# Performance work log

Hardware: AMD Instinct MI355X
Metric: run time of the kernel (lower is better)

Reference implementation:

```python
import jax, jax.numpy as jnp
import numpy as np

N_NODES = 100000
N_EDGES = 1600000
IN_DIM, HID, OUT_DIM = 128, 64, 1


def _sage_conv(x, src, dst, wl, wr, b, num_nodes):
    # PyG SAGEConv (aggr='mean', root_weight=True):
    #   out = lin_l(mean_{j in N(i)} x_j) + lin_r(x_i), bias lives in lin_l
    msgs = x[src]                                                  # [E, d] gather
    agg = jax.ops.segment_sum(msgs, dst, num_segments=num_nodes)  # [N, d]
    deg = jax.ops.segment_sum(jnp.ones((src.shape[0],), x.dtype), dst,
                              num_segments=num_nodes)              # [N]
    agg = agg / jnp.maximum(deg, 1.0)[:, None]                     # mean aggregation
    return agg @ wl + x @ wr + b


def setup_inputs() -> dict:
    key = jax.random.key(0)
    ks = jax.random.split(key, 12)
    x = jax.random.normal(ks[0], (N_NODES, IN_DIM), dtype=jnp.float32)
    edge_index = jax.random.randint(ks[1], (2, N_EDGES), 0, N_NODES, dtype=jnp.int64)

    def glorot(k, fan_in, fan_out):
        s = jnp.sqrt(2.0 / (fan_in + fan_out)).astype(jnp.float32)
        return jax.random.normal(k, (fan_in, fan_out), dtype=jnp.float32) * s

    return {
        "x": x,
        "edge_index": edge_index,
        "wl0": glorot(ks[2], IN_DIM, HID), "wr0": glorot(ks[3], IN_DIM, HID),
        "b0": jnp.zeros((HID,), jnp.float32),
        "wl1": glorot(ks[4], HID, HID), "wr1": glorot(ks[5], HID, HID),
        "b1": jnp.zeros((HID,), jnp.float32),
        "wl2": glorot(ks[6], HID, OUT_DIM), "wr2": glorot(ks[7], HID, OUT_DIM),
        "b2": jnp.zeros((OUT_DIM,), jnp.float32),
    }


def reference(x, edge_index, wl0, wr0, b0, wl1, wr1, b1, wl2, wr2, b2):
    src, dst = edge_index[0], edge_index[1]
    n = x.shape[0]
    # layer 0: conv -> relu (dropout is identity in eval mode)
    h = jax.nn.relu(_sage_conv(x, src, dst, wl0, wr0, b0, n))
    # layer 1
    h = jax.nn.relu(_sage_conv(h, src, dst, wl1, wr1, b1, n))
    # final layer + sigmoid
    h = _sage_conv(h, src, dst, wl2, wr2, b2, n)
    return jax.nn.sigmoid(h)
```

## Files before the change

### kernel.cpp

```cpp
#include <hip/hip_runtime.h>
#include <hip/hip_bf16.h>
#include <math.h>


#define SHIFT 7
#define BKT 128
#define CHUNK 4096

typedef __bf16 bf16_t;
typedef bf16_t bf16x8 __attribute__((ext_vector_type(8)));
typedef float f32x4 __attribute__((ext_vector_type(4)));

__global__ __launch_bounds__(256) void hist_bucket(const int* __restrict__ dstv,
                                                   int* __restrict__ bucket_cnt,
                                                   int E, int NB, int nbC,
                                                   const float* __restrict__ wl0,
                                                   const float* __restrict__ wr0,
                                                   const float* __restrict__ wl1,
                                                   const float* __restrict__ wr1,
                                                   bf16_t* __restrict__ w0t,
                                                   bf16_t* __restrict__ w1t) {
    if ((int)blockIdx.x >= nbC) {
        int idx = (blockIdx.x - nbC) * 256 + threadIdx.x;
        if (idx < 128 * 128) {
            int j = idx >> 7, k = idx & 127;
            float v = (j < 64) ? wl0[k * 64 + j] : wr0[k * 64 + (j - 64)];
            w0t[idx] = (bf16_t)v;
        } else if (idx < 128 * 128 + 128 * 64) {
            int i2 = idx - 128 * 128;
            int j = i2 >> 6, k = i2 & 63;
            float v = (j < 64) ? wl1[k * 64 + j] : wr1[k * 64 + (j - 64)];
            w1t[i2] = (bf16_t)v;
        }
        return;
    }
    __shared__ int h[1024];
    for (int i = threadIdx.x; i < NB; i += 256) h[i] = 0;
    __syncthreads();
    int base = blockIdx.x * CHUNK;
#pragma unroll
    for (int k = 0; k < CHUNK / 256; ++k) {
        int e = base + threadIdx.x + k * 256;
        if (e < E) atomicAdd(&h[dstv[e] >> SHIFT], 1);
    }
    __syncthreads();
    for (int i = threadIdx.x; i < NB; i += 256)
        if (h[i]) atomicAdd(&bucket_cnt[i], h[i]);
}

__global__ __launch_bounds__(1024) void scan_bucket(const int* __restrict__ cnt,
                                                    int* __restrict__ boff,
                                                    int* __restrict__ bcur, int NB) {
    __shared__ int s[1024];
    int t = threadIdx.x;
    int v = (t < NB) ? cnt[t] : 0;
    s[t] = v;
    __syncthreads();
    for (int d = 1; d < 1024; d <<= 1) {
        int x = (t >= d) ? s[t - d] : 0;
        __syncthreads();
        s[t] += x;
        __syncthreads();
    }
    if (t < NB) {
        int o = s[t] - v;
        boff[t] = o;
        bcur[t] = o;
    }
    if (t == NB - 1) boff[NB] = s[t];
}

__global__ __launch_bounds__(256) void scatter_bucket(const int* __restrict__ srcv,
                                                      const int* __restrict__ dstv,
                                                      int* __restrict__ bcur,
                                                      int* __restrict__ bucketed,
                                                      int E, int NB) {
    __shared__ int hist[1024];
    __shared__ int offl[1024];
    __shared__ int basel[1024];
    __shared__ int partial[256];
    __shared__ int posA[CHUNK];
    __shared__ int valA[CHUNK];
    const int t = threadIdx.x;
    for (int i = t; i < NB; i += 256) hist[i] = 0;
    __syncthreads();

    const int cbase = blockIdx.x * CHUNK;
    int bk[CHUNK / 256], rk[CHUNK / 256], vv[CHUNK / 256];
#pragma unroll
    for (int k = 0; k < CHUNK / 256; ++k) {
        int e = cbase + t + k * 256;
        if (e < E) {
            int d = dstv[e];
            int s = srcv[e];
            int b = d >> SHIFT;
            bk[k] = b;
            rk[k] = atomicAdd(&hist[b], 1);
            vv[k] = (s << SHIFT) | (d & (BKT - 1));
        } else {
            bk[k] = -1;
        }
    }
    __syncthreads();

    for (int b = t; b < NB; b += 256) {
        int c = hist[b];
        basel[b] = c ? atomicAdd(&bcur[b], c) : 0;
    }
    {
        int g = t * 4;
        int a0 = (g + 0 < NB) ? hist[g + 0] : 0;
        int a1 = (g + 1 < NB) ? hist[g + 1] : 0;
        int a2 = (g + 2 < NB) ? hist[g + 2] : 0;
        int a3 = (g + 3 < NB) ? hist[g + 3] : 0;
        int sum = a0 + a1 + a2 + a3;
        partial[t] = sum;
        __syncthreads();
        for (int d = 1; d < 256; d <<= 1) {
            int x = (t >= d) ? partial[t - d] : 0;
            __syncthreads();
            partial[t] += x;
            __syncthreads();
        }
        int ex = partial[t] - sum;
        if (g + 0 < NB) offl[g + 0] = ex;
        if (g + 1 < NB) offl[g + 1] = ex + a0;
        if (g + 2 < NB) offl[g + 2] = ex + a0 + a1;
        if (g + 3 < NB) offl[g + 3] = ex + a0 + a1 + a2;
    }
    __syncthreads();

    int nloc = E - cbase;
    if (nloc > CHUNK) nloc = CHUNK;
#pragma unroll
    for (int k = 0; k < CHUNK / 256; ++k) {
        if (bk[k] >= 0) {
            int slot = offl[bk[k]] + rk[k];
            posA[slot] = basel[bk[k]] + rk[k];
            valA[slot] = vv[k];
        }
    }
    __syncthreads();
    for (int j = t; j < nloc; j += 256) bucketed[posA[j]] = valA[j];
}

__global__ __launch_bounds__(256) void sort_bucket(const int* __restrict__ bucketed,
                                                   const int* __restrict__ boff,
                                                   int2* __restrict__ od,
                                                   int* __restrict__ csr, int N) {
    __shared__ int cnt[BKT];
    __shared__ int sc[BKT];
    __shared__ int cur[BKT];
    const int b = blockIdx.x;
    const int t = threadIdx.x;
    const int ebase = boff[b], eend = boff[b + 1];
    if (t < BKT) cnt[t] = 0;
    __syncthreads();
    for (int i = ebase + t; i < eend; i += 256)
        atomicAdd(&cnt[bucketed[i] & (BKT - 1)], 1);
    __syncthreads();
    int v = (t < BKT) ? cnt[t] : 0;
    if (t < BKT) sc[t] = v;
    __syncthreads();
    for (int d = 1; d < BKT; d <<= 1) {
        int x = (t < BKT && t >= d) ? sc[t - d] : 0;
        __syncthreads();
        if (t < BKT) sc[t] += x;
        __syncthreads();
    }
    if (t < BKT) {
        int ex = sc[t] - v;
        cur[t] = ex;
        int dst = (b << SHIFT) + t;
        if (dst < N) od[dst] = make_int2(ebase + ex, v);
    }
    __syncthreads();
    for (int i = ebase + t; i < eend; i += 256) {
        int w = bucketed[i];
        int p = atomicAdd(&cur[w & (BKT - 1)], 1);
        csr[ebase + p] = w >> SHIFT;
    }
}

template <int KTOT, bool AIN_BF16>
__global__ __launch_bounds__(256) void gemm_mfma(const void* __restrict__ Ain,
                                                 const bf16_t* __restrict__ Wt,
                                                 bf16_t* __restrict__ Y, int N) {
    const int lane = threadIdx.x & 63;
    const int wv = threadIdx.x >> 6;
    const int r0 = blockIdx.x * 64 + wv * 16;
    const int rr = lane & 15;
    const int quad = lane >> 4;
    const int row_store = r0 + rr;
    int row = (row_store < N) ? row_store : (N - 1);
    constexpr int NK = KTOT / 32;

    bf16x8 xf[NK];
    if (AIN_BF16) {
        const bf16_t* A = (const bf16_t*)Ain;
#pragma unroll
        for (int kk = 0; kk < NK; ++kk)
            xf[kk] = *(const bf16x8*)&A[(size_t)row * KTOT + kk * 32 + quad * 8];
    } else {
        const float* A = (const float*)Ain;
#pragma unroll
        for (int kk = 0; kk < NK; ++kk) {
            const float* ap = &A[(size_t)row * KTOT + kk * 32 + quad * 8];
            float4 f0 = *(const float4*)ap;
            float4 f1 = *(const float4*)(ap + 4);
            union { bf16x8 v; bf16_t h[8]; } u;
            u.h[0] = (bf16_t)f0.x; u.h[1] = (bf16_t)f0.y;
            u.h[2] = (bf16_t)f0.z; u.h[3] = (bf16_t)f0.w;
            u.h[4] = (bf16_t)f1.x; u.h[5] = (bf16_t)f1.y;
            u.h[6] = (bf16_t)f1.z; u.h[7] = (bf16_t)f1.w;
            xf[kk] = u.v;
        }
    }

#pragma unroll
    for (int c = 0; c < 8; ++c) {
        f32x4 acc = {0.f, 0.f, 0.f, 0.f};
#pragma unroll
        for (int kk = 0; kk < NK; ++kk) {
            bf16x8 wf = *(const bf16x8*)&Wt[(size_t)(c * 16 + rr) * KTOT + kk * 32 + quad * 8];
            acc = __builtin_amdgcn_mfma_f32_16x16x32_bf16(wf, xf[kk], acc, 0, 0, 0);
        }
        if (row_store < N) {
            union { bf16_t h[4]; uint2 u; } p;
            p.h[0] = (bf16_t)acc[0]; p.h[1] = (bf16_t)acc[1];
            p.h[2] = (bf16_t)acc[2]; p.h[3] = (bf16_t)acc[3];
            *(uint2*)&Y[(size_t)row_store * 128 + c * 16 + quad * 4] = p.u;
        }
    }
}

template <bool FUSED>
__global__ __launch_bounds__(256) void agg_relu(const bf16_t* __restrict__ y,
                                                const int* __restrict__ csr,
                                                const int2* __restrict__ od,
                                                const float* __restrict__ bias,
                                                bf16_t* __restrict__ h,
                                                const float* __restrict__ wl2,
                                                const float* __restrict__ wr2,
                                                float* __restrict__ sl,
                                                float* __restrict__ sr, int N) {
    int wid = blockIdx.x * 4 + (threadIdx.x >> 6);
    if (wid >= N) return;
    const int lane = threadIdx.x & 63;
    const int half = lane >> 5;
    const int ch = (lane & 31) * 2;
    const int2 odv = od[wid];
    const int base = odv.x;
    const int d = odv.y;

    int sidx = (lane < d) ? csr[base + lane] : 0;

    int lastLane = (d > 0 && d - 1 < 64) ? (d - 1) : 0;
    int s_last = __shfl(sidx, lastLane);

    float ax = 0.f, ay = 0.f;
    const int npairs = d >> 1;
    const int pm = (npairs < 32) ? npairs : 32;
    int p = 0;
    for (; p + 8 <= pm; p += 8) {
        int s[8];
#pragma unroll
        for (int j = 0; j < 8; ++j) s[j] = __shfl(sidx, 2 * (p + j) + half);
        uint v[8];
#pragma unroll
        for (int j = 0; j < 8; ++j) v[j] = *(const uint*)&y[(size_t)s[j] * 128 + ch];
#pragma unroll
        for (int j = 0; j < 8; ++j) {
            ax += __uint_as_float(v[j] << 16);
            ay += __uint_as_float(v[j] & 0xffff0000u);
        }
    }
    for (; p < pm; ++p) {
        int s0 = __shfl(sidx, 2 * p + half);
        uint v0 = *(const uint*)&y[(size_t)s0 * 128 + ch];
        ax += __uint_as_float(v0 << 16);
        ay += __uint_as_float(v0 & 0xffff0000u);
    }
    for (; p < npairs; ++p) {
        int s0 = csr[base + 2 * p + half];
        uint v0 = *(const uint*)&y[(size_t)s0 * 128 + ch];
        ax += __uint_as_float(v0 << 16);
        ay += __uint_as_float(v0 & 0xffff0000u);
    }
    if ((d & 1) && half == 0) {
        int s0 = (d - 1 < 64) ? s_last : csr[base + d - 1];
        uint v0 = *(const uint*)&y[(size_t)s0 * 128 + ch];
        ax += __uint_as_float(v0 << 16);
        ay += __uint_as_float(v0 & 0xffff0000u);
    }
    ax += __shfl_xor(ax, 32);
    ay += __shfl_xor(ay, 32);

    float inv = 1.f / ((d > 0) ? (float)d : 1.f);
    uint vs = *(const uint*)&y[(size_t)wid * 128 + 64 + ch];
    float2 bv = *(const float2*)&bias[ch];
    float vx = fmaxf(ax * inv + __uint_as_float(vs << 16) + bv.x, 0.f);
    float vy = fmaxf(ay * inv + __uint_as_float(vs & 0xffff0000u) + bv.y, 0.f);

    if (!FUSED) {
        if (half == 0) {
            union { bf16_t b[2]; uint u; } pk;
            pk.b[0] = (bf16_t)vx;
            pk.b[1] = (bf16_t)vy;
            *(uint*)&h[(size_t)wid * 64 + ch] = pk.u;
        }
    } else {
        float a = vx * wl2[ch] + vy * wl2[ch + 1];
        float b = vx * wr2[ch] + vy * wr2[ch + 1];
#pragma unroll
        for (int off = 16; off; off >>= 1) {
            a += __shfl_xor(a, off);
            b += __shfl_xor(b, off);
        }
        if (lane == 0) {
            sl[wid] = a;
            sr[wid] = b;
        }
    }
}

__global__ __launch_bounds__(256) void final_k(const float* __restrict__ sl,
                                               const float* __restrict__ sr,
                                               const int* __restrict__ csr,
                                               const int2* __restrict__ od,
                                               const float* __restrict__ b2,
                                               float* __restrict__ out, int N) {
    int wid = blockIdx.x * 4 + (threadIdx.x >> 6);
    if (wid >= N) return;
    const int lane = threadIdx.x & 63;
    const int2 odv = od[wid];
    const int base = odv.x;
    const int d = odv.y;
    float acc = 0.f;
    for (int e = lane; e < d; e += 64) acc += sl[csr[base + e]];
#pragma unroll
    for (int off = 32; off; off >>= 1) acc += __shfl_xor(acc, off);
    if (lane == 0) {
        float m = (d > 0) ? (float)d : 1.f;
        float v = acc / m + sr[wid] + b2[0];
        out[wid] = 1.f / (1.f + expf(-v));
    }
}

extern "C" void kernel_launch(void* const* d_in, const int* in_sizes, int n_in,
                              void* d_out, int out_size, void* d_ws, size_t ws_size,
                              hipStream_t stream) {
    const float* x  = (const float*)d_in[0];
    const int*  ei  = (const int*)d_in[1];
    const float* wl0 = (const float*)d_in[2];
    const float* wr0 = (const float*)d_in[3];
    const float* b0  = (const float*)d_in[4];
    const float* wl1 = (const float*)d_in[5];
    const float* wr1 = (const float*)d_in[6];
    const float* b1  = (const float*)d_in[7];
    const float* wl2 = (const float*)d_in[8];
    const float* wr2 = (const float*)d_in[9];
    const float* b2  = (const float*)d_in[10];
    float* out = (float*)d_out;

    const int E = in_sizes[1] / 2;
    const int N = out_size;
    const int* srcv = ei;
    const int* dstv = ei + E;
    const int NB = (N + BKT - 1) >> SHIFT;

    char* ws = (char*)d_ws;
    size_t o = 0;
    auto take = [&](size_t nbytes) -> void* {
        void* p = ws + o;
        o = (o + nbytes + 255) & ~(size_t)255;
        return p;
    };
    int2* od    = (int2*)take((size_t)N * 8);
    int* bcnt   = (int*)take((size_t)(NB + 2) * 4);
    int* boff   = (int*)take((size_t)(NB + 2) * 4);
    int* bcur   = (int*)take((size_t)(NB + 2) * 4);
    int* csr    = (int*)take((size_t)E * 4);
    bf16_t* w0t = (bf16_t*)take(128 * 128 * 2);
    bf16_t* w1t = (bf16_t*)take(128 * 64 * 2);
    bf16_t* y   = (bf16_t*)take((size_t)N * 128 * 2);
    bf16_t* h   = (bf16_t*)take((size_t)N * 64 * 2);
    float* sl   = (float*)take((size_t)N * 4);
    float* sr   = (float*)take((size_t)N * 4);
    int* bucketed = (int*)y;
    (void)ws_size;

    const int nbC = (E + CHUNK - 1) / CHUNK;
    const int nbP = (128 * 128 + 128 * 64 + 255) / 256;
    const int nbW = (N + 3) / 4;
    const int nbG = (N + 63) / 64;

    hipMemsetAsync(bcnt, 0, (size_t)NB * 4, stream);
    hist_bucket<<<nbC + nbP, 256, 0, stream>>>(dstv, bcnt, E, NB, nbC,
                                               wl0, wr0, wl1, wr1, w0t, w1t);
    scan_bucket<<<1, 1024, 0, stream>>>(bcnt, boff, bcur, NB);
    scatter_bucket<<<nbC, 256, 0, stream>>>(srcv, dstv, bcur, bucketed, E, NB);
    sort_bucket<<<NB, 256, 0, stream>>>(bucketed, boff, od, csr, N);

    gemm_mfma<128, false><<<nbG, 256, 0, stream>>>((const void*)x, w0t, y, N);
    agg_relu<false><<<nbW, 256, 0, stream>>>(y, csr, od, b0, h,
                                             nullptr, nullptr, nullptr, nullptr, N);
    gemm_mfma<64, true><<<nbG, 256, 0, stream>>>((const void*)h, w1t, y, N);
    agg_relu<true><<<nbW, 256, 0, stream>>>(y, csr, od, b1, nullptr,
                                            wl2, wr2, sl, sr, N);
    final_k<<<nbW, 256, 0, stream>>>(sl, sr, csr, od, b2, out, N);
}
```

Baseline: 330.7 us.

## Use persistent grid-stride waves with 4 edges per step and prefetched CSR indices in aggregation

Rewrites agg_relu as a persistent kernel on 2048 blocks where each wave loops over nodes in grid-stride order. While it aggregates the current node, it prefetches the next node's offset/degree and neighbor indices. Lanes now split into quads that each handle one edge with 8-byte loads of 4 channels, so four edges are in flight per step instead of two. This aims to hide index-load latency and issue wider gathers. The cost is an extra cross-quad shuffle reduction and less parallelism per node.

```diff
diff --git a/kernel.cpp b/kernel.cpp
--- a/kernel.cpp
+++ b/kernel.cpp
@@ -234,6 +234,9 @@
     }
 }
 
+#define B16LO(u) __uint_as_float((u) << 16)
+#define B16HI(u) __uint_as_float((u) & 0xffff0000u)
+
 template <bool FUSED>
 __global__ __launch_bounds__(256) void agg_relu(const bf16_t* __restrict__ y,
                                                 const int* __restrict__ csr,
@@ -244,83 +247,106 @@
                                                 const float* __restrict__ wr2,
                                                 float* __restrict__ sl,
                                                 float* __restrict__ sr, int N) {
-    int wid = blockIdx.x * 4 + (threadIdx.x >> 6);
-    if (wid >= N) return;
     const int lane = threadIdx.x & 63;
-    const int half = lane >> 5;
-    const int ch = (lane & 31) * 2;
-    const int2 odv = od[wid];
-    const int base = odv.x;
-    const int d = odv.y;
-
-    int sidx = (lane < d) ? csr[base + lane] : 0;
-
-    int lastLane = (d > 0 && d - 1 < 64) ? (d - 1) : 0;
-    int s_last = __shfl(sidx, lastLane);
-
-    float ax = 0.f, ay = 0.f;
-    const int npairs = d >> 1;
-    const int pm = (npairs < 32) ? npairs : 32;
-    int p = 0;
-    for (; p + 8 <= pm; p += 8) {
-        int s[8];
-#pragma unroll
-        for (int j = 0; j < 8; ++j) s[j] = __shfl(sidx, 2 * (p + j) + half);
-        uint v[8];
-#pragma unroll
-        for (int j = 0; j < 8; ++j) v[j] = *(const uint*)&y[(size_t)s[j] * 128 + ch];
-#pragma unroll
-        for (int j = 0; j < 8; ++j) {
-            ax += __uint_as_float(v[j] << 16);
-            ay += __uint_as_float(v[j] & 0xffff0000u);
-        }
-    }
-    for (; p < pm; ++p) {
-        int s0 = __shfl(sidx, 2 * p + half);
-        uint v0 = *(const uint*)&y[(size_t)s0 * 128 + ch];
-        ax += __uint_as_float(v0 << 16);
-        ay += __uint_as_float(v0 & 0xffff0000u);
-    }
-    for (; p < npairs; ++p) {
-        int s0 = csr[base + 2 * p + half];
-        uint v0 = *(const uint*)&y[(size_t)s0 * 128 + ch];
-        ax += __uint_as_float(v0 << 16);
-        ay += __uint_as_float(v0 & 0xffff0000u);
-    }
-    if ((d & 1) && half == 0) {
-        int s0 = (d - 1 < 64) ? s_last : csr[base + d - 1];
-        uint v0 = *(const uint*)&y[(size_t)s0 * 128 + ch];
-        ax += __uint_as_float(v0 << 16);
-        ay += __uint_as_float(v0 & 0xffff0000u);
-    }
-    ax += __shfl_xor(ax, 32);
-    ay += __shfl_xor(ay, 32);
-
-    float inv = 1.f / ((d > 0) ? (float)d : 1.f);
-    uint vs = *(const uint*)&y[(size_t)wid * 128 + 64 + ch];
-    float2 bv = *(const float2*)&bias[ch];
-    float vx = fmaxf(ax * inv + __uint_as_float(vs << 16) + bv.x, 0.f);
-    float vy = fmaxf(ay * inv + __uint_as_float(vs & 0xffff0000u) + bv.y, 0.f);
-
-    if (!FUSED) {
-        if (half == 0) {
-            union { bf16_t b[2]; uint u; } pk;
-            pk.b[0] = (bf16_t)vx;
-            pk.b[1] = (bf16_t)vy;
-            *(uint*)&h[(size_t)wid * 64 + ch] = pk.u;
-        }
-    } else {
-        float a = vx * wl2[ch] + vy * wl2[ch + 1];
-        float b = vx * wr2[ch] + vy * wr2[ch + 1];
-#pragma unroll
-        for (int off = 16; off; off >>= 1) {
-            a += __shfl_xor(a, off);
-            b += __shfl_xor(b, off);
-        }
-        if (lane == 0) {
-            sl[wid] = a;
-            sr[wid] = b;
-        }
+    const int quad = lane >> 4;
+    const int ch = (lane & 15) * 4;
+    const int nw = gridDim.x * 4;
+
+    int i = blockIdx.x * 4 + (threadIdx.x >> 6);
+    int2 odc = (i < N) ? od[i] : make_int2(0, 0);
+    int sidx = 0;
+    if (i < N) sidx = (lane < odc.y) ? csr[odc.x + lane] : 0;
+
+    while (i < N) {
+        const int inext = i + nw;
+        int2 odn = (inext < N) ? od[inext] : make_int2(0, 0);
+
+        const int base = odc.x;
+        const int d = odc.y;
+        float a0 = 0.f, a1 = 0.f, a2 = 0.f, a3 = 0.f;
+        const int nblk = d >> 2;
+        const int pm = (nblk < 16) ? nblk : 16;
+        int p = 0;
+        for (; p + 4 <= pm; p += 4) {
+            int s0 = __shfl(sidx, 4 * p + quad);
+            int s1 = __shfl(sidx, 4 * p + 4 + quad);
+            int s2 = __shfl(sidx, 4 * p + 8 + quad);
+            int s3 = __shfl(sidx, 4 * p + 12 + quad);
+            uint2 v0 = *(const uint2*)&y[(size_t)s0 * 128 + ch];
+            uint2 v1 = *(const uint2*)&y[(size_t)s1 * 128 + ch];
+            uint2 v2 = *(const uint2*)&y[(size_t)s2 * 128 + ch];
+            uint2 v3 = *(const uint2*)&y[(size_t)s3 * 128 + ch];
+            a0 += B16LO(v0.x) + B16LO(v1.x) + B16LO(v2.x) + B16LO(v3.x);
+            a1 += B16HI(v0.x) + B16HI(v1.x) + B16HI(v2.x) + B16HI(v3.x);
+            a2 += B16LO(v0.y) + B16LO(v1.y) + B16LO(v2.y) + B16LO(v3.y);
+            a3 += B16HI(v0.y) + B16HI(v1.y) + B16HI(v2.y) + B16HI(v3.y);
+        }
+        for (; p < pm; ++p) {
+            int s0 = __shfl(sidx, 4 * p + quad);
+            uint2 v0 = *(const uint2*)&y[(size_t)s0 * 128 + ch];
+            a0 += B16LO(v0.x); a1 += B16HI(v0.x);
+            a2 += B16LO(v0.y); a3 += B16HI(v0.y);
+        }
+        for (; p < nblk; ++p) {
+            int s0 = csr[base + 4 * p + quad];
+            uint2 v0 = *(const uint2*)&y[(size_t)s0 * 128 + ch];
+            a0 += B16LO(v0.x); a1 += B16HI(v0.x);
+            a2 += B16LO(v0.y); a3 += B16HI(v0.y);
+        }
+        {
+            int te = 4 * nblk + quad;
+            int tec = (te < 64) ? te : 63;
+            int s_t = __shfl(sidx, tec);
+            if (te < d) {
+                int s0 = (te < 64) ? s_t : csr[base + te];
+                uint2 v0 = *(const uint2*)&y[(size_t)s0 * 128 + ch];
+                a0 += B16LO(v0.x); a1 += B16HI(v0.x);
+                a2 += B16LO(v0.y); a3 += B16HI(v0.y);
+            }
+        }
+
+        int sidxn = 0;
+        if (inext < N) sidxn = (lane < odn.y) ? csr[odn.x + lane] : 0;
+
+        a0 += __shfl_xor(a0, 16); a1 += __shfl_xor(a1, 16);
+        a2 += __shfl_xor(a2, 16); a3 += __shfl_xor(a3, 16);
+        a0 += __shfl_xor(a0, 32); a1 += __shfl_xor(a1, 32);
+        a2 += __shfl_xor(a2, 32); a3 += __shfl_xor(a3, 32);
+
+        float inv = 1.f / ((d > 0) ? (float)d : 1.f);
+        uint2 vs = *(const uint2*)&y[(size_t)i * 128 + 64 + ch];
+        float4 bv = *(const float4*)&bias[ch];
+        float vx0 = fmaxf(a0 * inv + B16LO(vs.x) + bv.x, 0.f);
+        float vx1 = fmaxf(a1 * inv + B16HI(vs.x) + bv.y, 0.f);
+        float vx2 = fmaxf(a2 * inv + B16LO(vs.y) + bv.z, 0.f);
+        float vx3 = fmaxf(a3 * inv + B16HI(vs.y) + bv.w, 0.f);
+
+        if (!FUSED) {
+            if (quad == 0) {
+                union { bf16_t b[4]; uint2 u; } pk;
+                pk.b[0] = (bf16_t)vx0; pk.b[1] = (bf16_t)vx1;
+                pk.b[2] = (bf16_t)vx2; pk.b[3] = (bf16_t)vx3;
+                *(uint2*)&h[(size_t)i * 64 + ch] = pk.u;
+            }
+        } else {
+            float4 wv = *(const float4*)&wl2[ch];
+            float4 wu = *(const float4*)&wr2[ch];
+            float a = vx0 * wv.x + vx1 * wv.y + vx2 * wv.z + vx3 * wv.w;
+            float b = vx0 * wu.x + vx1 * wu.y + vx2 * wu.z + vx3 * wu.w;
+#pragma unroll
+            for (int off = 8; off; off >>= 1) {
+                a += __shfl_xor(a, off);
+                b += __shfl_xor(b, off);
+            }
+            if (lane == 0) {
+                sl[i] = a;
+                sr[i] = b;
+            }
+        }
+
+        odc = odn;
+        sidx = sidxn;
+        i = inext;
     }
 }
 
@@ -394,6 +420,7 @@
     const int nbP = (128 * 128 + 128 * 64 + 255) / 256;
     const int nbW = (N + 3) / 4;
     const int nbG = (N + 63) / 64;
+    const int nbA = 2048;
 
     hipMemsetAsync(bcnt, 0, (size_t)NB * 4, stream);
     hist_bucket<<<nbC + nbP, 256, 0, stream>>>(dstv, bcnt, E, NB, nbC,
@@ -403,10 +430,10 @@
     sort_bucket<<<NB, 256, 0, stream>>>(bucketed, boff, od, csr, N);
 
     gemm_mfma<128, false><<<nbG, 256, 0, stream>>>((const void*)x, w0t, y, N);
-    agg_relu<false><<<nbW, 256, 0, stream>>>(y, csr, od, b0, h,
+    agg_relu<false><<<nbA, 256, 0, stream>>>(y, csr, od, b0, h,
                                              nullptr, nullptr, nullptr, nullptr, N);
     gemm_mfma<64, true><<<nbG, 256, 0, stream>>>((const void*)h, w1t, y, N);
-    agg_relu<true><<<nbW, 256, 0, stream>>>(y, csr, od, b1, nullptr,
+    agg_relu<true><<<nbA, 256, 0, stream>>>(y, csr, od, b1, nullptr,
                                             wl2, wr2, sl, sr, N);
     final_k<<<nbW, 256, 0, stream>>>(sl, sr, csr, od, b2, out, N);
 }
```

Result: faster. 314.5 us (-4.9%).
